# Optimization experiments

Hardware: AMD Instinct MI355X
Metric: run time of the kernel (lower is better)

The kernel has to match this reference:

```python
import jax, jax.numpy as jnp
import numpy as np

L, N, E, H, D, F = 2048, 2, 1024, 16, 64, 4096  # seq, batch, embed, heads, head_dim, ffn
EPS = 1e-5


def _ln(x, w, b):
    m = jnp.mean(x, axis=-1, keepdims=True)
    v = jnp.mean(jnp.square(x - m), axis=-1, keepdims=True)
    return (x - m) * jax.lax.rsqrt(v + EPS) * w + b


def setup_inputs() -> dict:
    key = jax.random.key(0)
    ks = jax.random.split(key, 16)
    s = 0.02
    f32 = jnp.float32
    return {
        "x": jax.random.normal(ks[0], (L, N, E), f32),
        "ln1_w": jnp.ones((E,), f32),
        "ln1_b": jnp.zeros((E,), f32),
        "wq": jax.random.normal(ks[1], (H * D, E), f32) * s,
        "bq": jnp.zeros((H * D,), f32),
        "wk": jax.random.normal(ks[2], (H * D, E), f32) * s,
        "bk": jnp.zeros((H * D,), f32),
        "wv": jax.random.normal(ks[3], (H * D, E), f32) * s,
        "bv": jnp.zeros((H * D,), f32),
        "wout": jax.random.normal(ks[4], (E, H * D), f32) * s,
        "bout": jnp.zeros((E,), f32),
        "ln2_w": jnp.ones((E,), f32),
        "ln2_b": jnp.zeros((E,), f32),
        "fc1_w": jax.random.normal(ks[5], (F, E), f32) * s,
        "fc1_b": jnp.zeros((F,), f32),
        "fc2_w": jax.random.normal(ks[6], (E, F), f32) * s,
        "fc2_b": jnp.zeros((E,), f32),
    }


def reference(x, ln1_w, ln1_b, wq, bq, wk, bk, wv, bv, wout, bout,
              ln2_w, ln2_b, fc1_w, fc1_b, fc2_w, fc2_b):
    scale = D ** (-0.5)
    residual = x
    h = _ln(x, ln1_w, ln1_b)                      # (L,N,E)
    q = (h @ wq.T + bq).reshape(L, N, H, D) * scale
    k = (h @ wk.T + bk).reshape(L, N, H, D)
    v = (h @ wv.T + bv).reshape(L, N, H, D)
    attn = jnp.einsum('qnhd,knhd->nhqk', q, k)    # (N,H,L,L) full score matrix
    causal = jnp.tril(jnp.ones((L, L), bool))
    attn = jnp.where(causal[None, None], attn, jnp.float32(-10000.0))
    p = jax.nn.softmax(attn, axis=-1)
    o = jnp.einsum('nhqk,knhd->qnhd', p, v).reshape(L, N, H * D)
    o = o @ wout.T + bout
    x = o + residual
    residual = x
    h = _ln(x, ln2_w, ln2_b)
    h = jax.nn.gelu(h @ fc1_w.T + fc1_b, approximate=False)
    h = h @ fc2_w.T + fc2_b
    return h + residual
```

## Files before the change

### kernel.cpp

```cpp
#include <hip/hip_runtime.h>
#include <hip/hip_bf16.h>
#include <math.h>

using bf16 = __hip_bfloat16;
typedef __bf16 bf16x8 __attribute__((ext_vector_type(8)));
typedef short  short4v __attribute__((ext_vector_type(4)));
typedef float  f32x4  __attribute__((ext_vector_type(4)));

static constexpr int Lq = 2048, Nb = 2, E = 1024, Hh = 16, Dd = 64, Ff = 4096;
static constexpr int MT = Lq * Nb;
static constexpr int QKLD = 2 * E;
static constexpr int LDL = 2 * QKLD;

__device__ __forceinline__ void async_lds16(const void* g, void* l) {
  __builtin_amdgcn_global_load_lds(
      (const __attribute__((address_space(1))) void*)g,
      (__attribute__((address_space(3))) void*)l, 16, 0, 0);
}
__device__ __forceinline__ bf16x8 ld8(const bf16* p) { return *(const bf16x8*)p; }
__device__ __forceinline__ short bfbits(float x) {
  bf16 t = __float2bfloat16(x);
  return *(short*)&t;
}
__device__ __forceinline__ float gelu_fast(float v) {
  const float y = fminf(2.302208f * (v + 0.044715f * v * v * v), 80.f);
  const float t = exp2f(y);
  return v * t / (t + 1.0f);
}

__global__ __launch_bounds__(256) void cvt_all_kernel(
    const float* __restrict__ wq, const float* __restrict__ wk,
    const float* __restrict__ wv, const float* __restrict__ wout,
    const float* __restrict__ fc1w, const float* __restrict__ fc2w,
    bf16* __restrict__ wqkvb, bf16* __restrict__ woutb,
    bf16* __restrict__ f1wb, bf16* __restrict__ f2wb) {
  const int i = blockIdx.x * 256 + threadIdx.x;
  const float* src;
  bf16* dst;
  size_t off;
  if (i < 786432) {
    const int r = i >> 18;
    off = (size_t)(i & 262143);
    src = (r == 0) ? wq : (r == 1) ? wk : wv;
    dst = wqkvb + (size_t)r * (E * E);
  } else if (i < 1048576) {
    off = (size_t)(i - 786432); src = wout; dst = woutb;
  } else if (i < 2097152) {
    off = (size_t)(i - 1048576); src = fc1w; dst = f1wb;
  } else {
    off = (size_t)(i - 2097152); src = fc2w; dst = f2wb;
  }
  float4 v = ((const float4*)src)[off];
  bf16 o4[4] = {__float2bfloat16(v.x), __float2bfloat16(v.y),
                __float2bfloat16(v.z), __float2bfloat16(v.w)};
  *(uint2*)(dst + 4 * off) = *(uint2*)o4;
}

template <int EPI, int BK>
__global__ __launch_bounds__(256) void gemm_bt(
    const bf16* __restrict__ A, const bf16* __restrict__ W,
    const float* __restrict__ b1, const float* __restrict__ b2,
    const float* __restrict__ b3, int Klen, int Kstride, int Nld,
    float qscale, int scut, bf16* __restrict__ outb,
    bf16* __restrict__ outv) {
  __shared__ __align__(16) bf16 As[128 * BK];
  __shared__ __align__(16) bf16 Bs[128 * BK];
  const int tid = threadIdx.x;
  const int w = tid >> 6, lane = tid & 63;
  const int quad = lane >> 4, l16 = lane & 15;
  const int wm = (w >> 1) * 64, wn = (w & 1) * 64;
  const int m0 = blockIdx.y * 128, n0 = blockIdx.x * 128;
  const int koff = blockIdx.z * Klen;

  f32x4 acc[4][4];
#pragma unroll
  for (int i = 0; i < 4; i++)
#pragma unroll
    for (int j = 0; j < 4; j++)
#pragma unroll
      for (int r = 0; r < 4; r++) acc[i][j][r] = 0.f;

  if constexpr (BK == 32) {
    const int c0 = w * 64 + lane;
    const int c1 = c0 + 256;
    const size_t arow0 = (size_t)(m0 + (c0 >> 2)), arow1 = (size_t)(m0 + (c1 >> 2));
    const size_t brow0 = (size_t)(n0 + (c0 >> 2)), brow1 = (size_t)(n0 + (c1 >> 2));
    const int col0 = (c0 & 3) * 8, col1 = (c1 & 3) * 8;
    bf16* ldsA0 = &As[(w * 64) * 8];
    bf16* ldsA1 = &As[(256 + w * 64) * 8];
    bf16* ldsB0 = &Bs[(w * 64) * 8];
    bf16* ldsB1 = &Bs[(256 + w * 64) * 8];

    const int nk = Klen >> 5;
    for (int kt = 0; kt < nk; ++kt) {
      const int k0 = koff + kt * 32;
      async_lds16(A + arow0 * Kstride + k0 + col0, ldsA0);
      async_lds16(A + arow1 * Kstride + k0 + col1, ldsA1);
      async_lds16(W + brow0 * Kstride + k0 + col0, ldsB0);
      async_lds16(W + brow1 * Kstride + k0 + col1, ldsB1);
      __syncthreads();
      bf16x8 a[4], b[4];
#pragma unroll
      for (int i = 0; i < 4; i++) {
        a[i] = ld8(&As[(wm + i * 16 + l16) * 32 + quad * 8]);
        b[i] = ld8(&Bs[(wn + i * 16 + l16) * 32 + quad * 8]);
      }
#pragma unroll
      for (int i = 0; i < 4; i++)
#pragma unroll
        for (int j = 0; j < 4; j++)
          acc[i][j] = __builtin_amdgcn_mfma_f32_16x16x32_bf16(a[i], b[j], acc[i][j], 0, 0, 0);
      __syncthreads();
    }
  } else {
    const int rowoff = w * 8 + (lane >> 3);
    const int colsw = (((lane & 7) ^ (lane >> 3)) << 3);

    const int nk = Klen >> 6;
    for (int kt = 0; kt < nk; ++kt) {
      const int k0 = koff + (kt << 6);
#pragma unroll
      for (int r = 0; r < 4; r++) {
        async_lds16(A + (size_t)(m0 + r * 32 + rowoff) * Kstride + k0 + colsw,
                    As + (size_t)(r * 256 + w * 64) * 8);
        async_lds16(W + (size_t)(n0 + r * 32 + rowoff) * Kstride + k0 + colsw,
                    Bs + (size_t)(r * 256 + w * 64) * 8);
      }
      __syncthreads();
#pragma unroll
      for (int ksub = 0; ksub < 2; ksub++) {
        const int gx = ksub * 4 + quad;
        bf16x8 a[4], b[4];
#pragma unroll
        for (int i = 0; i < 4; i++) {
          const int ra = wm + i * 16 + l16;
          const int rb = wn + i * 16 + l16;
          a[i] = ld8(&As[(size_t)(ra * 8 + (gx ^ (l16 & 7))) * 8]);
          b[i] = ld8(&Bs[(size_t)(rb * 8 + (gx ^ (l16 & 7))) * 8]);
        }
#pragma unroll
        for (int i = 0; i < 4; i++)
#pragma unroll
          for (int j = 0; j < 4; j++)
            acc[i][j] = __builtin_amdgcn_mfma_f32_16x16x32_bf16(a[i], b[j], acc[i][j], 0, 0, 0);
      }
      __syncthreads();
    }
  }

  const size_t zoff = (EPI == 3) ? (size_t)blockIdx.z * ((size_t)MT * E) : 0;
#pragma unroll
  for (int i = 0; i < 4; i++) {
    const int mrow = m0 + wm + i * 16 + quad * 4;
#pragma unroll
    for (int j = 0; j < 4; j++) {
      const int ncol = n0 + wn + j * 16 + l16;
      float bv = 0.f;
      if constexpr (EPI != 3) {
        if (b3 != nullptr) {
          bv = (ncol < 1024) ? b1[ncol]
               : (ncol < 2048) ? b2[ncol - 1024] : b3[ncol - 2048];
        } else {
          bv = b1[ncol];
        }
      }
      const float sc = (ncol < scut) ? qscale : 1.0f;
#pragma unroll
      for (int r = 0; r < 4; r++) {
        float v = (acc[i][j][r] + bv) * sc;
        if constexpr (EPI == 2) {
          outb[(size_t)(mrow + r) * Nld + ncol] = __float2bfloat16(gelu_fast(v));
        } else if constexpr (EPI == 3) {
          outb[zoff + (size_t)(mrow + r) * Nld + ncol] = __float2bfloat16(v);
        } else {
          if (ncol < 2048) {
            outb[(size_t)(mrow + r) * 2048 + ncol] = __float2bfloat16(v);
          } else {
            const int h = (ncol - 2048) >> 6, d = ncol & 63;
            const int tok = mrow + r, n = tok & 1, l = tok >> 1;
            outv[(size_t)((n * 16 + h) * 64 + d) * Lq + l] = __float2bfloat16(v);
          }
        }
      }
    }
  }
}

template <int S, int H>
__device__ __forceinline__ void load_frags256(const char* Ab, const char* Bb,
                                              const int (&aoff)[8], const int (&boff)[4],
                                              bf16x8 (&a)[4], bf16x8 (&b)[4]) {
#pragma unroll
  for (int i = 0; i < 4; i++) a[i] = ld8((const bf16*)(Ab + S * 16384 + aoff[H * 4 + i]));
#pragma unroll
  for (int j = 0; j < 4; j++) b[j] = ld8((const bf16*)(Bb + S * 16384 + boff[j]));
}

template <int H>
__device__ __forceinline__ void mfma256(const bf16x8 (&a)[4], const bf16x8 (&b)[4],
                                        f32x4 (&acc)[8][4]) {
#pragma unroll
  for (int i = 0; i < 4; i++)
#pragma unroll
    for (int j = 0; j < 4; j++)
      acc[H * 4 + i][j] =
          __builtin_amdgcn_mfma_f32_16x16x32_bf16(a[i], b[j], acc[H * 4 + i][j], 0, 0, 0);
}

template <int K, int NOUT>
__global__ __launch_bounds__(512, 2) void gemm256_gelu(
    const bf16* __restrict__ A, const bf16* __restrict__ W,
    const float* __restrict__ bias, bf16* __restrict__ out) {
  extern __shared__ char smem[];
  constexpr int NKT = K / 64;
  static_assert(NKT >= 2, "need >=2 K-tiles");
  const int tid = threadIdx.x;
  const int w = tid >> 6, lane = tid & 63;
  const int quad = lane >> 4, l16 = lane & 15;
  const int wr = w >> 2, wc = w & 3;
  const int m0 = blockIdx.y * 256, n0 = blockIdx.x * 256;

  const int o0 = tid << 4;
  const int o1 = o0 + 8192;
  const int r0 = o0 >> 6, r1 = o1 >> 6;
  const int c0 = ((((o0 >> 4) & 3) ^ ((o0 >> 7) & 3)) << 3);
  const int c1 = ((((o1 >> 4) & 3) ^ ((o1 >> 7) & 3)) << 3);
  const bf16* Ag0 = A + (size_t)(m0 + r0) * K + c0;
  const bf16* Ag1 = A + (size_t)(m0 + r1) * K + c1;
  const bf16* Wg0 = W + (size_t)(n0 + r0) * K + c0;
  const bf16* Wg1 = W + (size_t)(n0 + r1) * K + c1;
  const int ldsw = w << 10;

  int aoff[8], boff[4];
#pragma unroll
  for (int h = 0; h < 2; h++)
#pragma unroll
    for (int i = 0; i < 4; i++) {
      const int ra = wr * 128 + h * 64 + i * 16 + l16;
      aoff[h * 4 + i] = ra * 64 + ((quad ^ ((ra >> 1) & 3)) << 4);
    }
#pragma unroll
  for (int j = 0; j < 4; j++) {
    const int rb = wc * 64 + j * 16 + l16;
    boff[j] = rb * 64 + ((quad ^ ((rb >> 1) & 3)) << 4);
  }

  f32x4 acc[8][4];
#pragma unroll
  for (int i = 0; i < 8; i++)
#pragma unroll
    for (int j = 0; j < 4; j++)
#pragma unroll
      for (int r = 0; r < 4; r++) acc[i][j][r] = 0.f;

  {
    char* d = smem;
    async_lds16(Ag0, d + ldsw);
    async_lds16(Ag1, d + 8192 + ldsw);
    async_lds16(Wg0, d + 32768 + ldsw);
    async_lds16(Wg1, d + 32768 + 8192 + ldsw);
    async_lds16(Ag0 + 32, d + 16384 + ldsw);
    async_lds16(Ag1 + 32, d + 16384 + 8192 + ldsw);
    async_lds16(Wg0 + 32, d + 49152 + ldsw);
    async_lds16(Wg1 + 32, d + 49152 + 8192 + ldsw);
  }
  asm volatile("s_waitcnt vmcnt(4)" ::: "memory");
  __builtin_amdgcn_s_barrier();

  for (int kt = 0; kt < NKT; ++kt) {
    const char* Ab = smem + ((kt & 1) << 16);
    const char* Bb = Ab + 32768;
    char* Sd = smem + (((kt + 1) & 1) << 16);
    const int kn = (kt + 1) << 6;
    if (kt + 1 < NKT) {
      {
        bf16x8 a[4], b[4];
        load_frags256<0, 0>(Ab, Bb, aoff, boff, a, b);
        async_lds16(Ag0 + kn, Sd + ldsw);
        async_lds16(Ag1 + kn, Sd + 8192 + ldsw);
        __builtin_amdgcn_s_barrier();
        __builtin_amdgcn_s_setprio(1);
        mfma256<0>(a, b, acc);
        __builtin_amdgcn_s_setprio(0);
        __builtin_amdgcn_sched_barrier(0);
        __builtin_amdgcn_s_barrier();
      }
      {
        bf16x8 a[4], b[4];
        load_frags256<0, 1>(Ab, Bb, aoff, boff, a, b);
        async_lds16(Wg0 + kn, Sd + 32768 + ldsw);
        async_lds16(Wg1 + kn, Sd + 32768 + 8192 + ldsw);
        __builtin_amdgcn_s_barrier();
        __builtin_amdgcn_s_setprio(1);
        mfma256<1>(a, b, acc);
        __builtin_amdgcn_s_setprio(0);
        asm volatile("s_waitcnt vmcnt(4)" ::: "memory");
        __builtin_amdgcn_sched_barrier(0);
        __builtin_amdgcn_s_barrier();
      }
      {
        bf16x8 a[4], b[4];
        load_frags256<1, 0>(Ab, Bb, aoff, boff, a, b);
        async_lds16(Ag0 + kn + 32, Sd + 16384 + ldsw);
        async_lds16(Ag1 + kn + 32, Sd + 16384 + 8192 + ldsw);
        __builtin_amdgcn_s_barrier();
        __builtin_amdgcn_s_setprio(1);
        mfma256<0>(a, b, acc);
        __builtin_amdgcn_s_setprio(0);
        __builtin_amdgcn_sched_barrier(0);
        __builtin_amdgcn_s_barrier();
      }
      {
        bf16x8 a[4], b[4];
        load_frags256<1, 1>(Ab, Bb, aoff, boff, a, b);
        async_lds16(Wg0 + kn + 32, Sd + 49152 + ldsw);
        async_lds16(Wg1 + kn + 32, Sd + 49152 + 8192 + ldsw);
        __builtin_amdgcn_s_barrier();
        __builtin_amdgcn_s_setprio(1);
        mfma256<1>(a, b, acc);
        __builtin_amdgcn_s_setprio(0);
        asm volatile("s_waitcnt vmcnt(4)" ::: "memory");
        __builtin_amdgcn_sched_barrier(0);
        __builtin_amdgcn_s_barrier();
      }
    } else {
      {
        bf16x8 a[4], b[4];
        load_frags256<0, 0>(Ab, Bb, aoff, boff, a, b);
        __builtin_amdgcn_s_barrier();
        __builtin_amdgcn_s_setprio(1);
        mfma256<0>(a, b, acc);
        __builtin_amdgcn_s_setprio(0);
        __builtin_amdgcn_sched_barrier(0);
        __builtin_amdgcn_s_barrier();
      }
      {
        bf16x8 a[4], b[4];
        load_frags256<0, 1>(Ab, Bb, aoff, boff, a, b);
        __builtin_amdgcn_s_barrier();
        __builtin_amdgcn_s_setprio(1);
        mfma256<1>(a, b, acc);
        __builtin_amdgcn_s_setprio(0);
        asm volatile("s_waitcnt vmcnt(0)" ::: "memory");
        __builtin_amdgcn_sched_barrier(0);
        __builtin_amdgcn_s_barrier();
      }
      {
        bf16x8 a[4], b[4];
        load_frags256<1, 0>(Ab, Bb, aoff, boff, a, b);
        __builtin_amdgcn_s_barrier();
        __builtin_amdgcn_s_setprio(1);
        mfma256<0>(a, b, acc);
        __builtin_amdgcn_s_setprio(0);
        __builtin_amdgcn_sched_barrier(0);
        __builtin_amdgcn_s_barrier();
      }
      {
        bf16x8 a[4], b[4];
        load_frags256<1, 1>(Ab, Bb, aoff, boff, a, b);
        __builtin_amdgcn_s_barrier();
        __builtin_amdgcn_s_setprio(1);
        mfma256<1>(a, b, acc);
        __builtin_amdgcn_s_setprio(0);
      }
    }
  }

#pragma unroll
  for (int j = 0; j < 4; j++) {
    const int col = n0 + wc * 64 + j * 16 + l16;
    const float bv = bias[col];
#pragma unroll
    for (int mI = 0; mI < 8; mI++) {
      const int row = m0 + wr * 128 + mI * 16 + quad * 4;
#pragma unroll
      for (int r = 0; r < 4; r++) {
        out[(size_t)(row + r) * NOUT + col] =
            __float2bfloat16(gelu_fast(acc[mI][j][r] + bv));
      }
    }
  }
}

__global__ __launch_bounds__(256) void reduce2_kernel(
    const bf16* __restrict__ P, const float* __restrict__ bias,
    const float* __restrict__ res, float* __restrict__ out) {
  const int i = blockIdx.x * 256 + threadIdx.x;
  const size_t e0 = (size_t)i * 4;
  const int col = (int)(e0 & (E - 1));
  uint2 u0 = *(const uint2*)(P + e0);
  uint2 u1 = *(const uint2*)(P + (size_t)MT * E + e0);
  const bf16* p0 = (const bf16*)&u0;
  const bf16* p1 = (const bf16*)&u1;
  float4 b = *(const float4*)(bias + col);
  float4 r = *(const float4*)(res + e0);
  float4 o;
  o.x = (float)p0[0] + (float)p1[0] + b.x + r.x;
  o.y = (float)p0[1] + (float)p1[1] + b.y + r.y;
  o.z = (float)p0[2] + (float)p1[2] + b.z + r.z;
  o.w = (float)p0[3] + (float)p1[3] + b.w + r.w;
  *(float4*)(out + e0) = o;
}

__global__ __launch_bounds__(256) void redln_kernel(
    const bf16* __restrict__ P, const float* __restrict__ bias,
    const float* __restrict__ res, const float* __restrict__ wgt,
    const float* __restrict__ bia, float* __restrict__ x1,
    bf16* __restrict__ h2) {
  const int t = blockIdx.x, tid = threadIdx.x;
  const size_t base = (size_t)t * E;
  const int e0 = tid * 4;
  uint2 u0 = *(const uint2*)(P + base + e0);
  uint2 u1 = *(const uint2*)(P + (size_t)MT * E + base + e0);
  const bf16* p0 = (const bf16*)&u0;
  const bf16* p1 = (const bf16*)&u1;
  float4 b = *(const float4*)(bias + e0);
  float4 r = *(const float4*)(res + base + e0);
  float v4[4];
  v4[0] = (float)p0[0] + (float)p1[0] + b.x + r.x;
  v4[1] = (float)p0[1] + (float)p1[1] + b.y + r.y;
  v4[2] = (float)p0[2] + (float)p1[2] + b.z + r.z;
  v4[3] = (float)p0[3] + (float)p1[3] + b.w + r.w;
  *(float4*)(x1 + base + e0) = *(float4*)v4;

  float s = 0.f, ss = 0.f;
#pragma unroll
  for (int i = 0; i < 4; i++) { s += v4[i]; ss += v4[i] * v4[i]; }
  for (int off = 32; off > 0; off >>= 1) {
    s += __shfl_down(s, off, 64);
    ss += __shfl_down(ss, off, 64);
  }
  __shared__ float rs[4], rss[4], mv[2];
  const int w = tid >> 6;
  if ((tid & 63) == 0) { rs[w] = s; rss[w] = ss; }
  __syncthreads();
  if (tid == 0) {
    float S = rs[0] + rs[1] + rs[2] + rs[3];
    float SS = rss[0] + rss[1] + rss[2] + rss[3];
    float mean = S * (1.f / E);
    float var = SS * (1.f / E) - mean * mean;
    mv[0] = mean; mv[1] = rsqrtf(var + 1e-5f);
  }
  __syncthreads();
  const float mean = mv[0], rstd = mv[1];
  float4 wg = *(const float4*)(wgt + e0);
  float4 bb = *(const float4*)(bia + e0);
  bf16 o4[4];
  o4[0] = __float2bfloat16((v4[0] - mean) * rstd * wg.x + bb.x);
  o4[1] = __float2bfloat16((v4[1] - mean) * rstd * wg.y + bb.y);
  o4[2] = __float2bfloat16((v4[2] - mean) * rstd * wg.z + bb.z);
  o4[3] = __float2bfloat16((v4[3] - mean) * rstd * wg.w + bb.w);
  *(uint2*)(h2 + base + e0) = *(uint2*)o4;
}

__global__ __launch_bounds__(256) void ln_kernel(
    const float* __restrict__ x, const float* __restrict__ wgt,
    const float* __restrict__ bia, bf16* __restrict__ out) {
  const int t = blockIdx.x, tid = threadIdx.x;
  const size_t base = (size_t)t * E;
  float v4[4], s = 0.f, ss = 0.f;
#pragma unroll
  for (int i = 0; i < 4; i++) {
    float v = x[base + i * 256 + tid];
    v4[i] = v; s += v; ss += v * v;
  }
  for (int off = 32; off > 0; off >>= 1) {
    s += __shfl_down(s, off, 64);
    ss += __shfl_down(ss, off, 64);
  }
  __shared__ float rs[4], rss[4], mv[2];
  const int w = tid >> 6;
  if ((tid & 63) == 0) { rs[w] = s; rss[w] = ss; }
  __syncthreads();
  if (tid == 0) {
    float S = rs[0] + rs[1] + rs[2] + rs[3];
    float SS = rss[0] + rss[1] + rss[2] + rss[3];
    float mean = S * (1.f / E);
    float var = SS * (1.f / E) - mean * mean;
    mv[0] = mean; mv[1] = rsqrtf(var + 1e-5f);
  }
  __syncthreads();
  const float mean = mv[0], rstd = mv[1];
#pragma unroll
  for (int i = 0; i < 4; i++) {
    const int e = i * 256 + tid;
    float r = (v4[i] - mean) * rstd * wgt[e] + bia[e];
    out[base + e] = __float2bfloat16(r);
  }
}

__global__ __launch_bounds__(256) void attn_kernel(
    const bf16* __restrict__ QK, const bf16* __restrict__ VT,
    bf16* __restrict__ O) {
  __shared__ __align__(16) bf16 KB[2][512 * 8];
  __shared__ __align__(16) bf16 VB[2][512 * 8];
  const int tid = threadIdx.x;
  const int w = tid >> 6, lane = tid & 63, quad = lane >> 4, l16 = lane & 15;
  const int bid = blockIdx.x;
  const int x = bid & 7;
  const int m = (bid >> 3) & 31;
  const int g = bid >> 8;
  const int j = m >> 2;
  const int hh = (m & 3) * 8 + x;
  const int qt = (g == 0) ? j : (g == 1) ? (31 - j) : (g == 2) ? (j + 8) : (23 - j);
  const int n = hh >> 4, h = hh & 15;

  const bf16* Qp = QK + n * QKLD + h * Dd;
  const bf16* Kp = Qp + E;
  const bf16* Vp = VT + (size_t)hh * 64 * Lq;
  const int w8 = w * 8;

  const int ql = qt * 64 + w * 16 + l16;
  const bf16x8 aq0 = ld8(Qp + (size_t)ql * LDL + quad * 8);
  const bf16x8 aq1 = ld8(Qp + (size_t)ql * LDL + 32 + quad * 8);
  asm volatile("s_waitcnt vmcnt(0)" ::: "memory");

  async_lds16(Kp + (size_t)lane * LDL + w8, &KB[0][(size_t)(w * 64) * 8]);
  async_lds16(Kp + (size_t)lane * LDL + 32 + w8, &KB[0][(size_t)(256 + w * 64) * 8]);
  async_lds16(Vp + (size_t)lane * Lq + w8, &VB[0][(size_t)(w * 64) * 8]);
  async_lds16(Vp + (size_t)lane * Lq + 32 + w8, &VB[0][(size_t)(256 + w * 64) * 8]);

  f32x4 o_acc[4];
#pragma unroll
  for (int d = 0; d < 4; d++)
#pragma unroll
    for (int r = 0; r < 4; r++) o_acc[d][r] = 0.f;
  float m_run = -3e30f, l_run = 0.f;

  for (int kt = 0; kt <= qt; ++kt) {
    const bf16* KBb = KB[kt & 1];
    const bf16* VBb = VB[kt & 1];
    if (kt < qt) {
      const size_t kb2 = (size_t)(kt + 1) * 64;
      bf16* Kd = &KB[(kt & 1) ^ 1][0];
      bf16* Vd = &VB[(kt & 1) ^ 1][0];
      async_lds16(Kp + (size_t)(kb2 + lane) * LDL + w8, Kd + (size_t)(w * 64) * 8);
      async_lds16(Kp + (size_t)(kb2 + lane) * LDL + 32 + w8,
                  Kd + (size_t)(256 + w * 64) * 8);
      async_lds16(Vp + (size_t)lane * Lq + kb2 + w8, Vd + (size_t)(w * 64) * 8);
      async_lds16(Vp + (size_t)lane * Lq + kb2 + 32 + w8,
                  Vd + (size_t)(256 + w * 64) * 8);
      asm volatile("s_waitcnt vmcnt(4)" ::: "memory");
    } else {
      asm volatile("s_waitcnt vmcnt(0)" ::: "memory");
    }
    __builtin_amdgcn_s_barrier();

    f32x4 s[4];
    __builtin_amdgcn_s_setprio(1);
#pragma unroll
    for (int ks = 0; ks < 4; ks++) {
      const bf16x8 kc0 = ld8(&KBb[(size_t)((quad)*64 + ks * 16 + l16) * 8]);
      const bf16x8 kc1 = ld8(&KBb[(size_t)((4 + quad) * 64 + ks * 16 + l16) * 8]);
#pragma unroll
      for (int r = 0; r < 4; r++) s[ks][r] = 0.f;
      s[ks] = __builtin_amdgcn_mfma_f32_16x16x32_bf16(kc0, aq0, s[ks], 0, 0, 0);
      s[ks] = __builtin_amdgcn_mfma_f32_16x16x32_bf16(kc1, aq1, s[ks], 0, 0, 0);
    }
    __builtin_amdgcn_s_setprio(0);

    if (kt == qt) {
#pragma unroll
      for (int ks = 0; ks < 4; ks++) {
#pragma unroll
        for (int r = 0; r < 4; r++) {
          const int kg = kt * 64 + ks * 16 + quad * 4 + r;
          if (kg > ql) s[ks][r] = -14427.0f;
        }
      }
    }

    float tmax = s[0][0];
#pragma unroll
    for (int ks = 0; ks < 4; ks++)
#pragma unroll
      for (int r = 0; r < 4; r++) tmax = fmaxf(tmax, s[ks][r]);
    tmax = fmaxf(tmax, __shfl_xor(tmax, 16, 64));
    tmax = fmaxf(tmax, __shfl_xor(tmax, 32, 64));
    float mbase = m_run;
    if (__any(tmax - m_run > 8.0f)) {
      const float mnew = fmaxf(m_run, tmax);
      const float alpha = exp2f(m_run - mnew);
      m_run = mnew;
      mbase = mnew;
      l_run *= alpha;
#pragma unroll
      for (int d = 0; d < 4; d++)
#pragma unroll
        for (int r = 0; r < 4; r++) o_acc[d][r] *= alpha;
    }
    float rsum = 0.f;
    short4v pf[4];
#pragma unroll
    for (int ks = 0; ks < 4; ks++) {
#pragma unroll
      for (int r = 0; r < 4; r++) {
        const float pv = exp2f(s[ks][r] - mbase);
        rsum += pv;
        pf[ks][r] = bfbits(pv);
      }
    }
    rsum += __shfl_xor(rsum, 16, 64);
    rsum += __shfl_xor(rsum, 32, 64);
    l_run += rsum;

    __builtin_amdgcn_s_setprio(1);
#pragma unroll
    for (int d = 0; d < 4; d++) {
#pragma unroll
      for (int ks = 0; ks < 4; ks++) {
        const int gg = ks * 2 + (quad >> 1);
        const short4v av =
            *(const short4v*)&VBb[(size_t)(gg * 64 + d * 16 + l16) * 8 + (quad & 1) * 4];
        o_acc[d] = __builtin_amdgcn_mfma_f32_16x16x16bf16_1k(av, pf[ks], o_acc[d], 0, 0, 0);
      }
    }
    __builtin_amdgcn_s_setprio(0);

    __builtin_amdgcn_sched_barrier(0);
    __builtin_amdgcn_s_barrier();
  }

  const float inv_l = 1.f / fmaxf(l_run, 1e-30f);
  const size_t obase = (size_t)ql * (Nb * E) + (size_t)n * E + h * Dd;
#pragma unroll
  for (int d = 0; d < 4; d++)
#pragma unroll
    for (int r = 0; r < 4; r++)
      O[obase + d * 16 + quad * 4 + r] = __float2bfloat16(o_acc[d][r] * inv_l);
}

extern "C" void kernel_launch(void* const* d_in, const int* in_sizes, int n_in,
                              void* d_out, int out_size, void* d_ws, size_t ws_size,
                              hipStream_t stream) {
  const float* x    = (const float*)d_in[0];
  const float* ln1w = (const float*)d_in[1];
  const float* ln1b = (const float*)d_in[2];
  const float* wq   = (const float*)d_in[3];
  const float* bq   = (const float*)d_in[4];
  const float* wk   = (const float*)d_in[5];
  const float* bk   = (const float*)d_in[6];
  const float* wv   = (const float*)d_in[7];
  const float* bv   = (const float*)d_in[8];
  const float* wout = (const float*)d_in[9];
  const float* bout = (const float*)d_in[10];
  const float* ln2w = (const float*)d_in[11];
  const float* ln2b = (const float*)d_in[12];
  const float* fc1w = (const float*)d_in[13];
  const float* fc1b = (const float*)d_in[14];
  const float* fc2w = (const float*)d_in[15];
  const float* fc2b = (const float*)d_in[16];

  char* ws = (char*)d_ws;
  bf16* wqkvb = (bf16*)(ws);
  bf16* woutb = (bf16*)(ws + ((size_t)6 << 20));
  bf16* f1wb  = (bf16*)(ws + ((size_t)8 << 20));
  bf16* f2wb  = (bf16*)(ws + ((size_t)16 << 20));
  bf16* h1    = (bf16*)(ws + ((size_t)24 << 20));
  bf16* qk    = (bf16*)(ws + ((size_t)32 << 20));
  bf16* vtg   = (bf16*)(ws + ((size_t)48 << 20));
  bf16* o     = (bf16*)(ws + ((size_t)56 << 20));
  float* x1   = (float*)(ws + ((size_t)64 << 20));
  bf16* Pout  = (bf16*)(ws + ((size_t)32 << 20));
  bf16* P01   = (bf16*)(ws);
  bf16* f1    = (bf16*)(ws + ((size_t)32 << 20));
  bf16* h2    = h1;
  float* outp = (float*)d_out;

  static bool g_shmem_attr = false;
  if (!g_shmem_attr) {
    hipFuncSetAttribute(reinterpret_cast<const void*>(gemm256_gelu<1024, 4096>),
                        hipFuncAttributeMaxDynamicSharedMemorySize, 131072);
    g_shmem_attr = true;
  }

  cvt_all_kernel<<<12288, 256, 0, stream>>>(wq, wk, wv, wout, fc1w, fc2w,
                                            wqkvb, woutb, f1wb, f2wb);

  ln_kernel<<<MT, 256, 0, stream>>>(x, ln1w, ln1b, h1);

  dim3 gQKV(3 * E / 128, MT / 128);
  dim3 gE2(E / 128, MT / 128, 2);

  gemm_bt<4, 64><<<gQKV, 256, 0, stream>>>(h1, wqkvb, bq, bk, bv, E, E, 2048,
                                           0.125f * 1.44269504f, 1024, qk, vtg);

  attn_kernel<<<1024, 256, 0, stream>>>(qk, vtg, o);

  gemm_bt<3, 64><<<gE2, 256, 0, stream>>>(o, woutb, nullptr, nullptr, nullptr,
                                          E / 2, E, E, 1.f, 0, Pout, nullptr);
  redln_kernel<<<MT, 256, 0, stream>>>(Pout, bout, x, ln2w, ln2b, x1, h2);

  gemm256_gelu<1024, 4096><<<dim3(Ff / 256, MT / 256), 512, 131072, stream>>>(
      h2, f1wb, fc1b, f1);

  gemm_bt<3, 64><<<gE2, 256, 0, stream>>>(f1, f2wb, nullptr, nullptr, nullptr,
                                          Ff / 2, Ff, E, 1.f, 0, P01, nullptr);
  reduce2_kernel<<<MT * E / 1024, 256, 0, stream>>>(P01, fc2b, x1, outp);
}
```

Before: 368.9 us.

## Store K and V in LDS-tiled layout so attention loads contiguous tiles

The QKV GEMM epilogue now writes Q to its own compact buffer and writes K and V in a pre-tiled per-head layout matching the LDS fragment order, instead of a strided row-major Q|K buffer and a transposed V. The attention kernel then fetches each 64-key tile with fully contiguous 16-byte async loads rather than strided gathers across rows. This trades scattered stores in the GEMM epilogue for coalesced reads in the attention inner loop.

```diff
diff --git a/kernel.cpp b/kernel.cpp
--- a/kernel.cpp
+++ b/kernel.cpp
@@ -9,8 +9,6 @@
 
 static constexpr int Lq = 2048, Nb = 2, E = 1024, Hh = 16, Dd = 64, Ff = 4096;
 static constexpr int MT = Lq * Nb;
-static constexpr int QKLD = 2 * E;
-static constexpr int LDL = 2 * QKLD;
 
 __device__ __forceinline__ void async_lds16(const void* g, void* l) {
   __builtin_amdgcn_global_load_lds(
@@ -62,7 +60,7 @@
     const float* __restrict__ b1, const float* __restrict__ b2,
     const float* __restrict__ b3, int Klen, int Kstride, int Nld,
     float qscale, int scut, bf16* __restrict__ outb,
-    bf16* __restrict__ outv) {
+    bf16* __restrict__ outv, bf16* __restrict__ outk) {
   __shared__ __align__(16) bf16 As[128 * BK];
   __shared__ __align__(16) bf16 Bs[128 * BK];
   const int tid = threadIdx.x;
@@ -173,12 +171,19 @@
         } else if constexpr (EPI == 3) {
           outb[zoff + (size_t)(mrow + r) * Nld + ncol] = __float2bfloat16(v);
         } else {
-          if (ncol < 2048) {
-            outb[(size_t)(mrow + r) * 2048 + ncol] = __float2bfloat16(v);
+          const int tok = mrow + r, n = tok & 1, l = tok >> 1;
+          if (ncol < 1024) {
+            outb[(size_t)tok * 1024 + ncol] = __float2bfloat16(v);
+          } else if (ncol < 2048) {
+            const int h = (ncol - 1024) >> 6, d = ncol & 63;
+            const int hh = n * 16 + h;
+            outk[((((size_t)hh * 32 + (l >> 6)) * 8 + (d >> 3)) * 64 + (l & 63)) * 8 +
+                 (d & 7)] = __float2bfloat16(v);
           } else {
             const int h = (ncol - 2048) >> 6, d = ncol & 63;
-            const int tok = mrow + r, n = tok & 1, l = tok >> 1;
-            outv[(size_t)((n * 16 + h) * 64 + d) * Lq + l] = __float2bfloat16(v);
+            const int hh = n * 16 + h;
+            outv[((((size_t)hh * 32 + (l >> 6)) * 8 + ((l >> 3) & 7)) * 64 + d) * 8 +
+                 (l & 7)] = __float2bfloat16(v);
           }
         }
       }
@@ -490,8 +495,8 @@
 }
 
 __global__ __launch_bounds__(256) void attn_kernel(
-    const bf16* __restrict__ QK, const bf16* __restrict__ VT,
-    bf16* __restrict__ O) {
+    const bf16* __restrict__ Q1, const bf16* __restrict__ KT,
+    const bf16* __restrict__ VT, bf16* __restrict__ O) {
   __shared__ __align__(16) bf16 KB[2][512 * 8];
   __shared__ __align__(16) bf16 VB[2][512 * 8];
   const int tid = threadIdx.x;
@@ -505,20 +510,20 @@
   const int qt = (g == 0) ? j : (g == 1) ? (31 - j) : (g == 2) ? (j + 8) : (23 - j);
   const int n = hh >> 4, h = hh & 15;
 
-  const bf16* Qp = QK + n * QKLD + h * Dd;
-  const bf16* Kp = Qp + E;
-  const bf16* Vp = VT + (size_t)hh * 64 * Lq;
-  const int w8 = w * 8;
+  const bf16* Qp = Q1 + n * E + h * Dd;
+  const bf16* Kb = KT + (size_t)hh * 32 * 4096;
+  const bf16* Vb = VT + (size_t)hh * 32 * 4096;
+  const int so = w * 512 + lane * 8;
 
   const int ql = qt * 64 + w * 16 + l16;
-  const bf16x8 aq0 = ld8(Qp + (size_t)ql * LDL + quad * 8);
-  const bf16x8 aq1 = ld8(Qp + (size_t)ql * LDL + 32 + quad * 8);
+  const bf16x8 aq0 = ld8(Qp + (size_t)ql * 2048 + quad * 8);
+  const bf16x8 aq1 = ld8(Qp + (size_t)ql * 2048 + 32 + quad * 8);
   asm volatile("s_waitcnt vmcnt(0)" ::: "memory");
 
-  async_lds16(Kp + (size_t)lane * LDL + w8, &KB[0][(size_t)(w * 64) * 8]);
-  async_lds16(Kp + (size_t)lane * LDL + 32 + w8, &KB[0][(size_t)(256 + w * 64) * 8]);
-  async_lds16(Vp + (size_t)lane * Lq + w8, &VB[0][(size_t)(w * 64) * 8]);
-  async_lds16(Vp + (size_t)lane * Lq + 32 + w8, &VB[0][(size_t)(256 + w * 64) * 8]);
+  async_lds16(Kb + so, &KB[0][w * 512]);
+  async_lds16(Kb + 2048 + so, &KB[0][2048 + w * 512]);
+  async_lds16(Vb + so, &VB[0][w * 512]);
+  async_lds16(Vb + 2048 + so, &VB[0][2048 + w * 512]);
 
   f32x4 o_acc[4];
 #pragma unroll
@@ -531,15 +536,13 @@
     const bf16* KBb = KB[kt & 1];
     const bf16* VBb = VB[kt & 1];
     if (kt < qt) {
-      const size_t kb2 = (size_t)(kt + 1) * 64;
+      const size_t tb = (size_t)(kt + 1) * 4096;
       bf16* Kd = &KB[(kt & 1) ^ 1][0];
       bf16* Vd = &VB[(kt & 1) ^ 1][0];
-      async_lds16(Kp + (size_t)(kb2 + lane) * LDL + w8, Kd + (size_t)(w * 64) * 8);
-      async_lds16(Kp + (size_t)(kb2 + lane) * LDL + 32 + w8,
-                  Kd + (size_t)(256 + w * 64) * 8);
-      async_lds16(Vp + (size_t)lane * Lq + kb2 + w8, Vd + (size_t)(w * 64) * 8);
-      async_lds16(Vp + (size_t)lane * Lq + kb2 + 32 + w8,
-                  Vd + (size_t)(256 + w * 64) * 8);
+      async_lds16(Kb + tb + so, Kd + w * 512);
+      async_lds16(Kb + tb + 2048 + so, Kd + 2048 + w * 512);
+      async_lds16(Vb + tb + so, Vd + w * 512);
+      async_lds16(Vb + tb + 2048 + so, Vd + 2048 + w * 512);
       asm volatile("s_waitcnt vmcnt(4)" ::: "memory");
     } else {
       asm volatile("s_waitcnt vmcnt(0)" ::: "memory");
@@ -657,7 +660,8 @@
   bf16* f1wb  = (bf16*)(ws + ((size_t)8 << 20));
   bf16* f2wb  = (bf16*)(ws + ((size_t)16 << 20));
   bf16* h1    = (bf16*)(ws + ((size_t)24 << 20));
-  bf16* qk    = (bf16*)(ws + ((size_t)32 << 20));
+  bf16* qk1   = (bf16*)(ws + ((size_t)32 << 20));
+  bf16* ktg   = (bf16*)(ws + ((size_t)40 << 20));
   bf16* vtg   = (bf16*)(ws + ((size_t)48 << 20));
   bf16* o     = (bf16*)(ws + ((size_t)56 << 20));
   float* x1   = (float*)(ws + ((size_t)64 << 20));
@@ -683,18 +687,18 @@
   dim3 gE2(E / 128, MT / 128, 2);
 
   gemm_bt<4, 64><<<gQKV, 256, 0, stream>>>(h1, wqkvb, bq, bk, bv, E, E, 2048,
-                                           0.125f * 1.44269504f, 1024, qk, vtg);
-
-  attn_kernel<<<1024, 256, 0, stream>>>(qk, vtg, o);
+                                           0.125f * 1.44269504f, 1024, qk1, vtg, ktg);
+
+  attn_kernel<<<1024, 256, 0, stream>>>(qk1, ktg, vtg, o);
 
   gemm_bt<3, 64><<<gE2, 256, 0, stream>>>(o, woutb, nullptr, nullptr, nullptr,
-                                          E / 2, E, E, 1.f, 0, Pout, nullptr);
+                                          E / 2, E, E, 1.f, 0, Pout, nullptr, nullptr);
   redln_kernel<<<MT, 256, 0, stream>>>(Pout, bout, x, ln2w, ln2b, x1, h2);
 
   gemm256_gelu<1024, 4096><<<dim3(Ff / 256, MT / 256), 512, 131072, stream>>>(
       h2, f1wb, fc1b, f1);
 
   gemm_bt<3, 64><<<gE2, 256, 0, stream>>>(f1, f2wb, nullptr, nullptr, nullptr,
-                                          Ff / 2, Ff, E, 1.f, 0, P01, nullptr);
+                                          Ff / 2, Ff, E, 1.f, 0, P01, nullptr, nullptr);
   reduce2_kernel<<<MT * E / 1024, 256, 0, stream>>>(P01, fc2b, x1, outp);
 }
```

After: 371.5 us. About the same (+0.7%).
